# Kernel optimization log

Measured on AMD Instinct MI355X. Metric: run time of the kernel, lower is better.

## Reference

```python
import jax, jax.numpy as jnp
import numpy as np

N_QUBITS = 12
N_LAYERS = 6
OUT_FEATURES = 64
BATCH = 8192


def _apply_1q(state, mat, q, n):
    # state: [B, 2**n] complex64; mat: [2,2] (shared) or [B,2,2] (per-sample)
    B = state.shape[0]
    left = 2 ** q
    s = state.reshape(B, left, 2, -1)
    if mat.ndim == 2:
        s = jnp.einsum('ab,Blbr->Blar', mat, s)
    else:
        s = jnp.einsum('Bab,Blbr->Blar', mat, s)
    return s.reshape(B, -1)


def _apply_cnot_adjacent(state, q, n):
    # CNOT with control q, target q+1 (adjacent wires): flip target where control=1
    B = state.shape[0]
    left = 2 ** q
    s = state.reshape(B, left, 2, 2, -1)
    s = jnp.stack([s[:, :, 0], s[:, :, 1, ::-1]], axis=2)
    return s.reshape(B, -1)


def _ry_mats(theta):
    # theta: [...] -> [..., 2, 2] RY matrices (real-valued rotation)
    c = jnp.cos(theta * 0.5)
    s = jnp.sin(theta * 0.5)
    row0 = jnp.stack([c, -s], axis=-1)
    row1 = jnp.stack([s, c], axis=-1)
    return jnp.stack([row0, row1], axis=-2).astype(jnp.complex64)


def _rot_mats(w):
    # w: [..., 3] = (phi, theta, omega); Rot = RZ(omega) @ RY(theta) @ RZ(phi)
    phi, theta, omega = w[..., 0], w[..., 1], w[..., 2]
    c = jnp.cos(theta * 0.5).astype(jnp.complex64)
    s = jnp.sin(theta * 0.5).astype(jnp.complex64)
    m00 = jnp.exp(-0.5j * (phi + omega)) * c
    m01 = -jnp.exp(0.5j * (phi - omega)) * s
    m10 = jnp.exp(0.5j * (omega - phi)) * s
    m11 = jnp.exp(0.5j * (phi + omega)) * c
    row0 = jnp.stack([m00, m01], axis=-1)
    row1 = jnp.stack([m10, m11], axis=-1)
    return jnp.stack([row0, row1], axis=-2)


def _circuit(x, params):
    # x: [B, n_qubits] angles, params: [L, n_qubits, 3]
    B = x.shape[0]
    n = N_QUBITS
    state = jnp.zeros((B, 2 ** n), jnp.complex64).at[:, 0].set(1.0)
    # data-encoding RY gates (per-sample matrices)
    ry = _ry_mats(x)  # [B, n, 2, 2]
    for q in range(n):
        state = _apply_1q(state, ry[:, q], q, n)
    # variational layers
    rot = _rot_mats(params)  # [L, n, 2, 2]
    for l in range(N_LAYERS):
        for q in range(n):
            state = _apply_1q(state, rot[l, q], q, n)
        for q in range(n - 1):
            state = _apply_cnot_adjacent(state, q, n)
    # <Z_q> for each qubit
    probs = state.real ** 2 + state.imag ** 2  # [B, 2**n]
    zs = []
    for q in range(n):
        p = probs.reshape(B, 2 ** q, 2, -1).sum(axis=(1, 3))  # [B, 2]
        zs.append(p[:, 0] - p[:, 1])
    return jnp.stack(zs, axis=-1).astype(jnp.float32)  # [B, n]


def setup_inputs() -> dict:
    key = jax.random.key(0)
    k1, k2, k3, k4 = jax.random.split(key, 4)
    x = jax.random.normal(k1, (BATCH, N_QUBITS), jnp.float32)
    params = jax.random.normal(k2, (N_LAYERS, N_QUBITS, 3), jnp.float32)
    bound = 1.0 / np.sqrt(N_QUBITS)
    W = jax.random.uniform(k3, (OUT_FEATURES, N_QUBITS), jnp.float32, -bound, bound)
    b = jax.random.uniform(k4, (OUT_FEATURES,), jnp.float32, -bound, bound)
    return {"x": x, "params": params, "W": W, "b": b}


def reference(x, params, W, b):
    q_out = _circuit(x, params)          # [B, n_qubits]
    return q_out @ W.T + b               # [B, out_features]
```

## Files before the change

### kernel.cpp

```cpp
#include <hip/hip_runtime.h>
#include <math.h>

typedef _Float16 h8 __attribute__((ext_vector_type(8)));
typedef float f4 __attribute__((ext_vector_type(4)));
typedef unsigned int u32;

#define BATCH 8192

#define SWZA(i) ((i) ^ (((((i) >> 4) ^ ((i) >> 7) ^ ((i) >> 10)) & 7) << 1))

__global__ void build_mats(const float* __restrict__ params, _Float16* __restrict__ ws) {
  int s = blockIdx.x, layer = s / 3, axis = s % 3;
  int t = threadIdx.x, n = t >> 4, col = t & 15;
  double Er = 1.0, Ei = 0.0;
  #pragma unroll
  for (int j = 0; j < 4; ++j) {
    int q = (axis == 0) ? (11 - j) : (axis == 1) ? (7 - j) : (3 - j);
    const float* pp = params + (layer * 12 + q) * 3;
    double phi = pp[0], th = pp[1], om = pp[2];
    double c = cos(0.5 * th), sn = sin(0.5 * th);
    double aa = 0.5 * (phi + om), bb = 0.5 * (phi - om);
    int nb = (n >> j) & 1, cb = (col >> j) & 1;
    double mr, mi;
    if (!nb) {
      if (!cb) { mr =  cos(aa) * c;  mi = -sin(aa) * c; }
      else     { mr = -cos(bb) * sn; mi = -sin(bb) * sn; }
    } else {
      if (!cb) { mr =  cos(bb) * sn; mi = -sin(bb) * sn; }
      else     { mr =  cos(aa) * c;  mi =  sin(aa) * c; }
    }
    double nr = Er * mr - Ei * mi, ni = Er * mi + Ei * mr;
    Er = nr; Ei = ni;
  }
  int a_;
  if (axis == 0 && layer > 0) {
    int kb = col >> 2, ll = col & 3;
    a_ = kb * 4 + ((ll ^ (ll >> 1)) ^ ((kb & 1) << 1));
  } else a_ = col;
  _Float16* reh = ws + s * 2048;
  _Float16* rel = reh + 512;
  _Float16* imh = reh + 1024;
  _Float16* iml = reh + 1536;
  int o0 = n * 32 + 2 * a_, o1 = o0 + 1;
  float v;
  _Float16 h;
  v = (float)Er;  h = (_Float16)v; reh[o0] = h; rel[o0] = (_Float16)((v - (float)h) * 2048.f);
  v = (float)-Ei; h = (_Float16)v; reh[o1] = h; rel[o1] = (_Float16)((v - (float)h) * 2048.f);
  v = (float)Ei;  h = (_Float16)v; imh[o0] = h; iml[o0] = (_Float16)((v - (float)h) * 2048.f);
  v = (float)Er;  h = (_Float16)v; imh[o1] = h; iml[o1] = (_Float16)((v - (float)h) * 2048.f);
}

__global__ __launch_bounds__(256) void circuit_kernel(
    const float* __restrict__ x, const _Float16* __restrict__ mats,
    const float* __restrict__ W, const float* __restrict__ bias,
    float* __restrict__ out) {
  __shared__ __align__(16) float2 st[4096];
  __shared__ float red[64];

  const int b = blockIdx.x;
  const int tid = threadIdx.x;
  const int lane = tid & 63, w = tid >> 6;
  const int r = lane & 15, kb = lane >> 4;

  float cs[12], sn_[12];
  #pragma unroll
  for (int q = 0; q < 12; ++q) {
    float sv, cv;
    sincosf(0.5f * x[b * 12 + q], &sv, &cv);
    cs[11 - q] = cv; sn_[11 - q] = sv;
  }
  {
    int hb = (w << 6) | lane;
    float basep = 1.f;
    #pragma unroll
    for (int i = 0; i < 8; ++i) basep *= ((hb >> i) & 1) ? sn_[4 + i] : cs[4 + i];
    float p2[4], q2[4];
    #pragma unroll
    for (int v = 0; v < 4; ++v) {
      p2[v] = ((v & 1) ? sn_[0] : cs[0]) * ((v & 2) ? sn_[1] : cs[1]);
      q2[v] = ((v & 1) ? sn_[2] : cs[2]) * ((v & 2) ? sn_[3] : cs[3]) * basep;
    }
    #pragma unroll
    for (int g = 0; g < 4; ++g) {
      int idx = w * 1024 + lane * 16 + g * 4;
      float a0 = q2[g] * p2[0], a1 = q2[g] * p2[1];
      float a2 = q2[g] * p2[2], a3 = q2[g] * p2[3];
      *(float4*)&st[SWZA(idx)]     = make_float4(a0, 0.f, a1, 0.f);
      *(float4*)&st[SWZA(idx + 2)] = make_float4(a2, 0.f, a3, 0.f);
    }
  }
  __syncthreads();

  const int g4r = r ^ (r >> 1);
  const int kb0 = kb & 1, kb1 = kb >> 1, m0 = r & 1;
  const int ob = ((kb1 ^ m0) << 1) | (kb0 ^ kb1);

  for (int layer = 0; layer < 6; ++layer) {
    #pragma unroll
    for (int axis = 0; axis < 3; ++axis) {
      const _Float16* mb = mats + (layer * 3 + axis) * 2048;
      const int bo = r * 32 + kb * 8;
      h8 breh = *(const h8*)(mb + bo);
      h8 brel = *(const h8*)(mb + 512 + bo);
      h8 bimh = *(const h8*)(mb + 1024 + bo);
      h8 biml = *(const h8*)(mb + 1536 + bo);
      float4 pA[4], pB[4];
      const bool fold = (axis == 0) && (layer > 0);
      #pragma unroll
      for (int i = 0; i < 4; ++i) {
        int tile = w * 4 + i;
        int ridx;
        if (fold) {
          int oh = tile ^ (tile >> 1);
          int om = g4r ^ ((tile & 1) << 3);
          ridx = (oh << 8) | (om << 4) | (ob << 2);
        } else {
          ridx = (tile << 8) | (r << 4) | (kb << 2);
        }
        float4 ra = *(const float4*)&st[SWZA(ridx)];
        float4 rb = *(const float4*)&st[SWZA(ridx + 2)];
        float fv[8] = {ra.x, ra.y, ra.z, ra.w, rb.x, rb.y, rb.z, rb.w};
        h8 ahi, alo;
        #pragma unroll
        for (int j = 0; j < 8; ++j) {
          _Float16 h = (_Float16)fv[j];
          ahi[j] = h;
          alo[j] = (_Float16)((fv[j] - (float)h) * 2048.f);
        }
        f4 mr = {0.f, 0.f, 0.f, 0.f}, mi = {0.f, 0.f, 0.f, 0.f};
        f4 cr = {0.f, 0.f, 0.f, 0.f}, ci = {0.f, 0.f, 0.f, 0.f};
        mr = __builtin_amdgcn_mfma_f32_16x16x32_f16(ahi, breh, mr, 0, 0, 0);
        cr = __builtin_amdgcn_mfma_f32_16x16x32_f16(alo, breh, cr, 0, 0, 0);
        cr = __builtin_amdgcn_mfma_f32_16x16x32_f16(ahi, brel, cr, 0, 0, 0);
        mi = __builtin_amdgcn_mfma_f32_16x16x32_f16(ahi, bimh, mi, 0, 0, 0);
        ci = __builtin_amdgcn_mfma_f32_16x16x32_f16(alo, bimh, ci, 0, 0, 0);
        ci = __builtin_amdgcn_mfma_f32_16x16x32_f16(ahi, biml, ci, 0, 0, 0);
        const float sc = 1.f / 2048.f;
        pA[i] = make_float4(fmaf(cr[0], sc, mr[0]), fmaf(ci[0], sc, mi[0]),
                            fmaf(cr[1], sc, mr[1]), fmaf(ci[1], sc, mi[1]));
        pB[i] = make_float4(fmaf(cr[2], sc, mr[2]), fmaf(ci[2], sc, mi[2]),
                            fmaf(cr[3], sc, mr[3]), fmaf(ci[3], sc, mi[3]));
      }
      __syncthreads();
      #pragma unroll
      for (int i = 0; i < 4; ++i) {
        int tile = w * 4 + i;
        int widx = (r << 8) | (tile << 4) | (kb << 2);
        *(float4*)&st[SWZA(widx)]     = pA[i];
        *(float4*)&st[SWZA(widx + 2)] = pB[i];
      }
      __syncthreads();
    }
  }

  float psum = 0.f, A0 = 0.f, A1 = 0.f, A2 = 0.f, A3 = 0.f;
  #pragma unroll
  for (int g = 0; g < 4; ++g) {
    int idx = w * 1024 + lane * 16 + g * 4;
    float4 ra = *(const float4*)&st[SWZA(idx)];
    float4 rb = *(const float4*)&st[SWZA(idx + 2)];
    float re_[4] = {ra.x, ra.z, rb.x, rb.z};
    float im_[4] = {ra.y, ra.w, rb.y, rb.w};
    #pragma unroll
    for (int j = 0; j < 4; ++j) {
      int tt = g * 4 + j;
      float p = re_[j] * re_[j] + im_[j] * im_[j];
      psum += p;
      A0 += (__builtin_popcount((unsigned)tt) & 1) ? -p : p;
      A1 += (__builtin_popcount((unsigned)(tt >> 1)) & 1) ? -p : p;
      A2 += (__builtin_popcount((unsigned)(tt >> 2)) & 1) ? -p : p;
      A3 += (__builtin_popcount((unsigned)(tt >> 3)) & 1) ? -p : p;
    }
  }
  float zs[12];
  {
    int u = (w << 6) | lane;
    int pu = __builtin_popcount((unsigned)u) & 1;
    zs[11] = pu ? -A0 : A0;
    zs[10] = pu ? -A1 : A1;
    zs[9]  = pu ? -A2 : A2;
    zs[8]  = pu ? -A3 : A3;
    #pragma unroll
    for (int q = 0; q <= 7; ++q) {
      int sgn = __builtin_popcount((unsigned)(u >> (7 - q))) & 1;
      zs[q] = sgn ? -psum : psum;
    }
  }
  #pragma unroll
  for (int q = 0; q < 12; ++q) {
    float v = zs[q];
    #pragma unroll
    for (int off = 1; off < 64; off <<= 1) v += __shfl_xor(v, off, 64);
    zs[q] = v;
  }
  if (lane == 0) {
    #pragma unroll
    for (int q = 0; q < 12; ++q) red[w * 12 + q] = zs[q];
  }
  __syncthreads();
  if (tid < 12) red[48 + tid] = red[tid] + red[12 + tid] + red[24 + tid] + red[36 + tid];
  __syncthreads();
  if (tid < 64) {
    float acc = bias[tid];
    #pragma unroll
    for (int q = 0; q < 12; ++q) acc = fmaf(red[48 + q], W[tid * 12 + q], acc);
    out[b * 64 + tid] = acc;
  }
}

extern "C" void kernel_launch(void* const* d_in, const int* in_sizes, int n_in,
                              void* d_out, int out_size, void* d_ws, size_t ws_size,
                              hipStream_t stream) {
  const float* x      = (const float*)d_in[0];
  const float* params = (const float*)d_in[1];
  const float* W      = (const float*)d_in[2];
  const float* bias   = (const float*)d_in[3];
  float* out = (float*)d_out;
  _Float16* mats = (_Float16*)d_ws;

  build_mats<<<18, 256, 0, stream>>>(params, mats);
  circuit_kernel<<<BATCH, 256, 0, stream>>>(x, mats, W, bias, out);
}
```

Measured before the change: 362.1 us.

## Fuse first two axis transforms per layer in registers, skipping an LDS round trip

Each layer's first two 4-qubit axis transforms are now chained in registers: the MFMA output of the first, re-split into hi/lo fp16, is fed straight into the second MFMA set. This only works if the accumulator layout of the first matches the operand layout the second needs. It drops one shared-memory write/read and two barriers per layer, and the store pattern after the fused pair changes to scalar float2 writes. Launch bounds now also request 4 blocks per CU, which may cap register use and cause spills, since more B-matrix fragments are live at once.

```diff
diff --git a/kernel.cpp b/kernel.cpp
--- a/kernel.cpp
+++ b/kernel.cpp
@@ -3,7 +3,6 @@
 
 typedef _Float16 h8 __attribute__((ext_vector_type(8)));
 typedef float f4 __attribute__((ext_vector_type(4)));
-typedef unsigned int u32;
 
 #define BATCH 8192
 
@@ -50,7 +49,7 @@
   v = (float)Er;  h = (_Float16)v; imh[o1] = h; iml[o1] = (_Float16)((v - (float)h) * 2048.f);
 }
 
-__global__ __launch_bounds__(256) void circuit_kernel(
+__global__ __launch_bounds__(256, 4) void circuit_kernel(
     const float* __restrict__ x, const _Float16* __restrict__ mats,
     const float* __restrict__ W, const float* __restrict__ bias,
     float* __restrict__ out) {
@@ -94,63 +93,121 @@
   const int g4r = r ^ (r >> 1);
   const int kb0 = kb & 1, kb1 = kb >> 1, m0 = r & 1;
   const int ob = ((kb1 ^ m0) << 1) | (kb0 ^ kb1);
+  const int bo = r * 32 + kb * 8;
+  const float sc = 1.f / 2048.f;
 
   for (int layer = 0; layer < 6; ++layer) {
-    #pragma unroll
-    for (int axis = 0; axis < 3; ++axis) {
-      const _Float16* mb = mats + (layer * 3 + axis) * 2048;
-      const int bo = r * 32 + kb * 8;
-      h8 breh = *(const h8*)(mb + bo);
-      h8 brel = *(const h8*)(mb + 512 + bo);
-      h8 bimh = *(const h8*)(mb + 1024 + bo);
-      h8 biml = *(const h8*)(mb + 1536 + bo);
-      float4 pA[4], pB[4];
-      const bool fold = (axis == 0) && (layer > 0);
-      #pragma unroll
-      for (int i = 0; i < 4; ++i) {
-        int tile = w * 4 + i;
-        int ridx;
-        if (fold) {
-          int oh = tile ^ (tile >> 1);
-          int om = g4r ^ ((tile & 1) << 3);
-          ridx = (oh << 8) | (om << 4) | (ob << 2);
-        } else {
-          ridx = (tile << 8) | (r << 4) | (kb << 2);
-        }
-        float4 ra = *(const float4*)&st[SWZA(ridx)];
-        float4 rb = *(const float4*)&st[SWZA(ridx + 2)];
-        float fv[8] = {ra.x, ra.y, ra.z, ra.w, rb.x, rb.y, rb.z, rb.w};
-        h8 ahi, alo;
-        #pragma unroll
-        for (int j = 0; j < 8; ++j) {
-          _Float16 h = (_Float16)fv[j];
-          ahi[j] = h;
-          alo[j] = (_Float16)((fv[j] - (float)h) * 2048.f);
-        }
-        f4 mr = {0.f, 0.f, 0.f, 0.f}, mi = {0.f, 0.f, 0.f, 0.f};
-        f4 cr = {0.f, 0.f, 0.f, 0.f}, ci = {0.f, 0.f, 0.f, 0.f};
-        mr = __builtin_amdgcn_mfma_f32_16x16x32_f16(ahi, breh, mr, 0, 0, 0);
-        cr = __builtin_amdgcn_mfma_f32_16x16x32_f16(alo, breh, cr, 0, 0, 0);
-        cr = __builtin_amdgcn_mfma_f32_16x16x32_f16(ahi, brel, cr, 0, 0, 0);
-        mi = __builtin_amdgcn_mfma_f32_16x16x32_f16(ahi, bimh, mi, 0, 0, 0);
-        ci = __builtin_amdgcn_mfma_f32_16x16x32_f16(alo, bimh, ci, 0, 0, 0);
-        ci = __builtin_amdgcn_mfma_f32_16x16x32_f16(ahi, biml, ci, 0, 0, 0);
-        const float sc = 1.f / 2048.f;
-        pA[i] = make_float4(fmaf(cr[0], sc, mr[0]), fmaf(ci[0], sc, mi[0]),
-                            fmaf(cr[1], sc, mr[1]), fmaf(ci[1], sc, mi[1]));
-        pB[i] = make_float4(fmaf(cr[2], sc, mr[2]), fmaf(ci[2], sc, mi[2]),
-                            fmaf(cr[3], sc, mr[3]), fmaf(ci[3], sc, mi[3]));
-      }
-      __syncthreads();
-      #pragma unroll
-      for (int i = 0; i < 4; ++i) {
-        int tile = w * 4 + i;
-        int widx = (r << 8) | (tile << 4) | (kb << 2);
-        *(float4*)&st[SWZA(widx)]     = pA[i];
-        *(float4*)&st[SWZA(widx + 2)] = pB[i];
-      }
-      __syncthreads();
-    }
+    const _Float16* mbL = mats + (layer * 3 + 0) * 2048;
+    const _Float16* mbM = mats + (layer * 3 + 1) * 2048;
+    h8 LbRh = *(const h8*)(mbL + bo),        LbRl = *(const h8*)(mbL + 512 + bo);
+    h8 LbIh = *(const h8*)(mbL + 1024 + bo), LbIl = *(const h8*)(mbL + 1536 + bo);
+    h8 MbRh = *(const h8*)(mbM + bo),        MbRl = *(const h8*)(mbM + 512 + bo);
+    h8 MbIh = *(const h8*)(mbM + 1024 + bo), MbIl = *(const h8*)(mbM + 1536 + bo);
+    float2 pend[4][4];
+    const bool fold = (layer > 0);
+    #pragma unroll
+    for (int i = 0; i < 4; ++i) {
+      int tile = w * 4 + i;
+      int ridx;
+      if (fold) {
+        int oh = tile ^ (tile >> 1);
+        int om = g4r ^ ((tile & 1) << 3);
+        ridx = (oh << 8) | (om << 4) | (ob << 2);
+      } else {
+        ridx = (tile << 8) | (r << 4) | (kb << 2);
+      }
+      float4 ra = *(const float4*)&st[SWZA(ridx)];
+      float4 rb = *(const float4*)&st[SWZA(ridx + 2)];
+      float fv[8] = {ra.x, ra.y, ra.z, ra.w, rb.x, rb.y, rb.z, rb.w};
+      h8 ahi, alo;
+      #pragma unroll
+      for (int j = 0; j < 8; ++j) {
+        _Float16 h = (_Float16)fv[j];
+        ahi[j] = h;
+        alo[j] = (_Float16)((fv[j] - (float)h) * 2048.f);
+      }
+      f4 mr = {0.f,0.f,0.f,0.f}, mi = {0.f,0.f,0.f,0.f};
+      f4 cr = {0.f,0.f,0.f,0.f}, ci = {0.f,0.f,0.f,0.f};
+      mr = __builtin_amdgcn_mfma_f32_16x16x32_f16(ahi, LbRh, mr, 0, 0, 0);
+      cr = __builtin_amdgcn_mfma_f32_16x16x32_f16(alo, LbRh, cr, 0, 0, 0);
+      cr = __builtin_amdgcn_mfma_f32_16x16x32_f16(ahi, LbRl, cr, 0, 0, 0);
+      mi = __builtin_amdgcn_mfma_f32_16x16x32_f16(ahi, LbIh, mi, 0, 0, 0);
+      ci = __builtin_amdgcn_mfma_f32_16x16x32_f16(alo, LbIh, ci, 0, 0, 0);
+      ci = __builtin_amdgcn_mfma_f32_16x16x32_f16(ahi, LbIl, ci, 0, 0, 0);
+      h8 bhi, blo;
+      #pragma unroll
+      for (int j = 0; j < 4; ++j) {
+        float gr = fmaf(cr[j], sc, mr[j]);
+        float gi = fmaf(ci[j], sc, mi[j]);
+        _Float16 hr = (_Float16)gr, hm = (_Float16)gi;
+        bhi[2*j] = hr; bhi[2*j+1] = hm;
+        blo[2*j]   = (_Float16)((gr - (float)hr) * 2048.f);
+        blo[2*j+1] = (_Float16)((gi - (float)hm) * 2048.f);
+      }
+      f4 nr = {0.f,0.f,0.f,0.f}, ni = {0.f,0.f,0.f,0.f};
+      f4 dr = {0.f,0.f,0.f,0.f}, di = {0.f,0.f,0.f,0.f};
+      nr = __builtin_amdgcn_mfma_f32_16x16x32_f16(bhi, MbRh, nr, 0, 0, 0);
+      dr = __builtin_amdgcn_mfma_f32_16x16x32_f16(blo, MbRh, dr, 0, 0, 0);
+      dr = __builtin_amdgcn_mfma_f32_16x16x32_f16(bhi, MbRl, dr, 0, 0, 0);
+      ni = __builtin_amdgcn_mfma_f32_16x16x32_f16(bhi, MbIh, ni, 0, 0, 0);
+      di = __builtin_amdgcn_mfma_f32_16x16x32_f16(blo, MbIh, di, 0, 0, 0);
+      di = __builtin_amdgcn_mfma_f32_16x16x32_f16(bhi, MbIl, di, 0, 0, 0);
+      #pragma unroll
+      for (int j = 0; j < 4; ++j)
+        pend[i][j] = make_float2(fmaf(dr[j], sc, nr[j]), fmaf(di[j], sc, ni[j]));
+    }
+    __syncthreads();
+    #pragma unroll
+    for (int i = 0; i < 4; ++i) {
+      int tile = w * 4 + i;
+      #pragma unroll
+      for (int j = 0; j < 4; ++j) {
+        int amp = (r << 8) | ((4 * kb + j) << 4) | tile;
+        st[SWZA(amp)] = pend[i][j];
+      }
+    }
+    __syncthreads();
+
+    const _Float16* mbH = mats + (layer * 3 + 2) * 2048;
+    h8 HbRh = *(const h8*)(mbH + bo),        HbRl = *(const h8*)(mbH + 512 + bo);
+    h8 HbIh = *(const h8*)(mbH + 1024 + bo), HbIl = *(const h8*)(mbH + 1536 + bo);
+    float4 pA[4], pB[4];
+    #pragma unroll
+    for (int i = 0; i < 4; ++i) {
+      int tile = w * 4 + i;
+      int ridx = (tile << 8) | (r << 4) | (kb << 2);
+      float4 ra = *(const float4*)&st[SWZA(ridx)];
+      float4 rb = *(const float4*)&st[SWZA(ridx + 2)];
+      float fv[8] = {ra.x, ra.y, ra.z, ra.w, rb.x, rb.y, rb.z, rb.w};
+      h8 ahi, alo;
+      #pragma unroll
+      for (int j = 0; j < 8; ++j) {
+        _Float16 h = (_Float16)fv[j];
+        ahi[j] = h;
+        alo[j] = (_Float16)((fv[j] - (float)h) * 2048.f);
+      }
+      f4 mr = {0.f,0.f,0.f,0.f}, mi = {0.f,0.f,0.f,0.f};
+      f4 cr = {0.f,0.f,0.f,0.f}, ci = {0.f,0.f,0.f,0.f};
+      mr = __builtin_amdgcn_mfma_f32_16x16x32_f16(ahi, HbRh, mr, 0, 0, 0);
+      cr = __builtin_amdgcn_mfma_f32_16x16x32_f16(alo, HbRh, cr, 0, 0, 0);
+      cr = __builtin_amdgcn_mfma_f32_16x16x32_f16(ahi, HbRl, cr, 0, 0, 0);
+      mi = __builtin_amdgcn_mfma_f32_16x16x32_f16(ahi, HbIh, mi, 0, 0, 0);
+      ci = __builtin_amdgcn_mfma_f32_16x16x32_f16(alo, HbIh, ci, 0, 0, 0);
+      ci = __builtin_amdgcn_mfma_f32_16x16x32_f16(ahi, HbIl, ci, 0, 0, 0);
+      pA[i] = make_float4(fmaf(cr[0], sc, mr[0]), fmaf(ci[0], sc, mi[0]),
+                          fmaf(cr[1], sc, mr[1]), fmaf(ci[1], sc, mi[1]));
+      pB[i] = make_float4(fmaf(cr[2], sc, mr[2]), fmaf(ci[2], sc, mi[2]),
+                          fmaf(cr[3], sc, mr[3]), fmaf(ci[3], sc, mi[3]));
+    }
+    __syncthreads();
+    #pragma unroll
+    for (int i = 0; i < 4; ++i) {
+      int tile = w * 4 + i;
+      int widx = (r << 8) | (tile << 4) | (kb << 2);
+      *(float4*)&st[SWZA(widx)]     = pA[i];
+      *(float4*)&st[SWZA(widx + 2)] = pB[i];
+    }
+    __syncthreads();
   }
 
   float psum = 0.f, A0 = 0.f, A1 = 0.f, A2 = 0.f, A3 = 0.f;
```

New measurement: 332.9 us. 8.0% less time.
